# Kernel optimization log

Hardware: AMD Instinct MI355X
Metric: run time of the kernel (lower is better)

## Reference

```python
import jax, jax.numpy as jnp
import numpy as np

B, CIN, COUT, H, W = 8, 128, 128, 64, 64

# kernel-grid base offsets (dy, dx), row-major k = kh*3 + kw, matching torch base_offset-1
BASE = jnp.array([[-1, -1], [-1, 0], [-1, 1],
                  [0, -1], [0, 0], [0, 1],
                  [1, -1], [1, 0], [1, 1]], dtype=jnp.float32)  # [9,2]
CORNER = jnp.array([1, 0, 1, 0, 0, 0, 1, 0, 1], dtype=jnp.float32)  # mask1 per kernel tap
EDGE = jnp.array([0, 1, 0, 1, 0, 1, 0, 1, 0], dtype=jnp.float32)    # mask2 per kernel tap


def conv3x3(x, w, b=None):
    out = jax.lax.conv_general_dilated(
        x, w, window_strides=(1, 1), padding=((1, 1), (1, 1)),
        dimension_numbers=('NCHW', 'OIHW', 'NCHW'))
    if b is not None:
        out = out + b[None, :, None, None]
    return out


def bilinear_sample(x, py, px):
    Bv, C, Hin, Win = x.shape
    y0 = jnp.floor(py)
    x0 = jnp.floor(px)
    wy = py - y0
    wx = px - x0
    y0i = y0.astype(jnp.int32)
    x0i = x0.astype(jnp.int32)
    xf = x.reshape(Bv, C, Hin * Win)

    def corner(yi, xi):
        valid = ((yi >= 0) & (yi < Hin) & (xi >= 0) & (xi < Win)).astype(x.dtype)
        idx = jnp.clip(yi, 0, Hin - 1) * Win + jnp.clip(xi, 0, Win - 1)  # [B,K,Ho,Wo]
        g = jax.vmap(lambda xb, ib: xb[:, ib])(xf, idx)  # [B,C,K,Ho,Wo]
        return g * valid[:, None]

    v00 = corner(y0i, x0i)
    v01 = corner(y0i, x0i + 1)
    v10 = corner(y0i + 1, x0i)
    v11 = corner(y0i + 1, x0i + 1)
    wy = wy[:, None]
    wx = wx[:, None]
    return (v00 * (1 - wy) * (1 - wx) + v01 * (1 - wy) * wx
            + v10 * wy * (1 - wx) + v11 * wy * wx)


def setup_inputs() -> dict:
    key = jax.random.key(0)
    k1, k2, k3 = jax.random.split(key, 3)
    x = jax.random.normal(k1, (B, CIN, H, W), dtype=jnp.float32)
    # small offset-conv weights keep predicted offsets in a realistic sub-pixel range
    w_off = jax.random.normal(k2, (5, CIN, 3, 3), dtype=jnp.float32) * 0.02
    b_off = jnp.zeros((5,), dtype=jnp.float32)
    w = jax.random.normal(k3, (COUT, CIN, 3, 3), dtype=jnp.float32) * (1.0 / np.sqrt(CIN * 9))
    b = jnp.zeros((COUT,), dtype=jnp.float32)
    return {"x": x, "w_off": w_off, "b_off": b_off, "w": w, "b": b}


def reference(x, w_off, b_off, w, b):
    off = conv3x3(x, w_off, b_off)          # [B,5,H,W]
    scale1 = jax.nn.relu(off[:, 2:3]) + 1.0  # corner scale [B,1,H,W]
    scale2 = jax.nn.relu(off[:, 3:4]) + 1.0  # edge scale   [B,1,H,W]
    shift = off[:, :2]                       # equivariant shift vector [B,2,H,W]

    # per-tap scale; center tap gets 0 but its base offset is (0,0) anyway
    scale_k = CORNER[None, :, None, None] * scale1 + EDGE[None, :, None, None] * scale2  # [B,9,H,W]
    # deform offset = scaled_base - base + shift = base*(scale-1) + shift
    delta = BASE[None, :, :, None, None] * (scale_k - 1.0)[:, :, None] + shift[:, None]  # [B,9,2,H,W]

    hs = jnp.arange(H, dtype=x.dtype)
    ws = jnp.arange(W, dtype=x.dtype)
    # sampling positions: p0 + base_k + offset_k (stride=1, pad=1)
    py = hs[None, None, :, None] + BASE[None, :, 0, None, None] + delta[:, :, 0]  # [B,9,H,W]
    px = ws[None, None, None, :] + BASE[None, :, 1, None, None] + delta[:, :, 1]

    sampled = bilinear_sample(x, py, px)  # [B,CIN,9,H,W]
    out = jnp.einsum('bckhw,ock->bohw', sampled, w.reshape(COUT, CIN, 9))
    return out + b[None, :, None, None]
```

## Files before the change

### kernel.cpp

```cpp
#include <hip/hip_runtime.h>

#define Wd 64
#define Hd 64
#define HWp 4096
#define CIN_ 128
#define COUT_ 128

typedef _Float16 f16;
typedef _Float16 h2    __attribute__((ext_vector_type(2)));
typedef _Float16 f16x8 __attribute__((ext_vector_type(8)));
typedef float f32x4    __attribute__((ext_vector_type(4)));

__device__ inline ushort f2h(float f) {
    f16 h = (f16)f;
    return __builtin_bit_cast(ushort, h);
}
__device__ inline h2 gb(const int4& g, int d) {
    return __builtin_bit_cast(h2, (&g.x)[d]);
}
__device__ inline h2 dup(float f) {
    f16 h = (f16)f;
    h2 r; r[0] = h; r[1] = h;
    return r;
}
struct H8 { h2 r[4]; };

__global__ __launch_bounds__(256) void prep_offsets_kernel(
    const float* __restrict__ x, const float* __restrict__ w,
    const float* __restrict__ w_off, const float* __restrict__ b_off,
    ushort* __restrict__ xt, ushort* __restrict__ w_t2,
    float4* __restrict__ der)
{
    __shared__ char smem[34816];
    int blk = blockIdx.x;
    int t = threadIdx.x;

    if (blk < 256) {
        ushort* tile = (ushort*)smem;
        int b = blk >> 5, yx0 = (blk & 31) << 7;
        const float* xb = x + (size_t)b * CIN_ * HWp + yx0;
        int lanelo = t & 31, grp = t >> 5;
        #pragma unroll
        for (int i = 0; i < 4; i++) {
            int cbase = i * 32 + grp * 4;
            float4 v0 = *(const float4*)(xb + (size_t)(cbase + 0) * HWp + lanelo * 4);
            float4 v1 = *(const float4*)(xb + (size_t)(cbase + 1) * HWp + lanelo * 4);
            float4 v2 = *(const float4*)(xb + (size_t)(cbase + 2) * HWp + lanelo * 4);
            float4 v3 = *(const float4*)(xb + (size_t)(cbase + 3) * HWp + lanelo * 4);
            ushort4 u;
            u.x = f2h(v0.x); u.y = f2h(v1.x); u.z = f2h(v2.x); u.w = f2h(v3.x);
            *(ushort4*)&tile[(lanelo * 4 + 0) * 136 + cbase] = u;
            u.x = f2h(v0.y); u.y = f2h(v1.y); u.z = f2h(v2.y); u.w = f2h(v3.y);
            *(ushort4*)&tile[(lanelo * 4 + 1) * 136 + cbase] = u;
            u.x = f2h(v0.z); u.y = f2h(v1.z); u.z = f2h(v2.z); u.w = f2h(v3.z);
            *(ushort4*)&tile[(lanelo * 4 + 2) * 136 + cbase] = u;
            u.x = f2h(v0.w); u.y = f2h(v1.w); u.z = f2h(v2.w); u.w = f2h(v3.w);
            *(ushort4*)&tile[(lanelo * 4 + 3) * 136 + cbase] = u;
        }
        __syncthreads();
        ushort* dst = xt + ((size_t)b * HWp + yx0) * CIN_;
        int c8 = (t & 15) * 8, yxg = t >> 4;
        #pragma unroll
        for (int i = 0; i < 8; i++) {
            int yxl = i * 16 + yxg;
            int4 v = *(int4*)&tile[yxl * 136 + c8];
            *(int4*)(dst + (size_t)yxl * CIN_ + c8) = v;
        }
    } else if (blk < 832) {
        int i = (blk - 256) * 256 + t;
        int j    = i & 7;
        int lane = (i >> 3) & 63;
        int ii   = (i >> 9) & 3;
        int wm   = (i >> 11) & 1;
        int s    = i >> 12;
        int o = wm * 64 + ii * 16 + (lane & 15);
        int c = (s & 3) * 32 + (lane >> 4) * 8 + j;
        int k = s >> 2;
        w_t2[i] = f2h(w[o * 1152 + c * 9 + k]);
    } else {
        float* wl   = (float*)smem;
        float* part = (float*)(smem + 18432);
        int blk2 = blk - 832;
        int b = blk2 >> 6;
        int h = blk2 & 63;

        for (int i = t; i < 4608; i += 256) {
            int j = i / 1152;
            int r = i - j * 1152;
            wl[r * 4 + j] = w_off[i];
        }
        __syncthreads();

        int pi = t & 63, cc = t >> 6;
        const float* xb = x + (size_t)(b * CIN_ + cc * 32) * HWp;

        int idx9[9];
        float msk9[9];
        #pragma unroll
        for (int dy = 0; dy < 3; dy++) {
            int hy = h + dy - 1;
            int hyc = min(max(hy, 0), Hd - 1);
            bool vr = (hy >= 0) && (hy < Hd);
            #pragma unroll
            for (int dx = 0; dx < 3; dx++) {
                int wx = pi + dx - 1;
                int wxc = min(max(wx, 0), Wd - 1);
                bool v = vr && (wx >= 0) && (wx < Wd);
                idx9[dy * 3 + dx] = hyc * Wd + wxc;
                msk9[dy * 3 + dx] = v ? 1.0f : 0.0f;
            }
        }

        float o0 = 0.f, o1 = 0.f, o2 = 0.f, o3 = 0.f;
        #pragma unroll 4
        for (int c = 0; c < 32; c++) {
            const float* xp = xb + c * HWp;
            const float* wc = &wl[(cc * 32 + c) * 36];
            float xv[9];
            #pragma unroll
            for (int tp = 0; tp < 9; tp++) xv[tp] = xp[idx9[tp]] * msk9[tp];
            #pragma unroll
            for (int tp = 0; tp < 9; tp++) {
                float4 wj = *(const float4*)&wc[tp * 4];
                o0 += xv[tp] * wj.x; o1 += xv[tp] * wj.y;
                o2 += xv[tp] * wj.z; o3 += xv[tp] * wj.w;
            }
        }
        part[t * 4 + 0] = o0;
        part[t * 4 + 1] = o1;
        part[t * 4 + 2] = o2;
        part[t * 4 + 3] = o3;
        __syncthreads();

        if (t < 64) {
            float s0 = b_off[0], s1 = b_off[1], s2 = b_off[2], s3 = b_off[3];
            #pragma unroll
            for (int q = 0; q < 4; q++) {
                s0 += part[(q * 64 + t) * 4 + 0];
                s1 += part[(q * 64 + t) * 4 + 1];
                s2 += part[(q * 64 + t) * 4 + 2];
                s3 += part[(q * 64 + t) * 4 + 3];
            }
            float4 d;
            d.x = s0;
            d.y = s1;
            d.z = fmaxf(s2, 0.f) + 1.f;
            d.w = fmaxf(s3, 0.f) + 1.f;
            der[(size_t)b * HWp + h * Wd + t] = d;
        }
    }
}

__global__ __launch_bounds__(256, 3) void deform_gemm_mfma(
    const ushort* __restrict__ xt, const ushort* __restrict__ w_t2,
    const float* __restrict__ bias, const float4* __restrict__ der,
    float* __restrict__ out)
{
    __shared__ ushort A_lds[2][2][4096];
    __shared__ int4 MI[9][64];
    __shared__ int4 MW[9][64];

    int t = threadIdx.x;
    int b = blockIdx.x & 7;
    int rp = blockIdx.x >> 3;
    int p0 = rp << 6;
    const char* xtb = (const char*)(xt + (size_t)b * HWp * CIN_);

    int wv = t >> 6, lane = t & 63;
    int lm = lane & 15, lq = lane >> 4;
    int myp = wv * 16 + lm;
    int lqb = lq * 16;

    f32x4 acc[8] = {};

    {
        int p = t >> 2;
        int pg = p0 + p;
        float fh = (float)(pg >> 6), fp = (float)(pg & 63);
        float4 dv = der[(size_t)b * HWp + pg];
        for (int k = (t & 3); k < 9; k += 4) {
            int ky = (k * 11) >> 5;
            int kx = k - ky * 3;
            float by = (float)(ky - 1), bx = (float)(kx - 1);
            bool corner = (ky != 1) && (kx != 1);
            bool edge = (ky != 1) ^ (kx != 1);
            float sk = corner ? dv.z : (edge ? dv.w : 0.0f);
            float py = fh + by * sk + dv.x;
            float px = fp + bx * sk + dv.y;
            float y0f = floorf(py), x0f = floorf(px);
            float wy = py - y0f, wx = px - x0f;
            int y0 = (int)y0f, x0 = (int)x0f;
            int y1 = y0 + 1, x1 = x0 + 1;
            float vy0 = (y0 >= 0 && y0 < Hd) ? 1.f : 0.f;
            float vy1 = (y1 >= 0 && y1 < Hd) ? 1.f : 0.f;
            float vx0 = (x0 >= 0 && x0 < Wd) ? 1.f : 0.f;
            float vx1 = (x1 >= 0 && x1 < Wd) ? 1.f : 0.f;
            int cy0 = min(max(y0, 0), Hd - 1), cy1 = min(max(y1, 0), Hd - 1);
            int cx0 = min(max(x0, 0), Wd - 1), cx1 = min(max(x1, 0), Wd - 1);
            int4 ii;
            ii.x = (cy0 * Wd + cx0) << 8;
            ii.y = (cy0 * Wd + cx1) << 8;
            ii.z = (cy1 * Wd + cx0) << 8;
            ii.w = (cy1 * Wd + cx1) << 8;
            MI[k][p] = ii;
            H8 hw;
            hw.r[0] = dup((1.f - wy) * (1.f - wx) * vy0 * vx0);
            hw.r[1] = dup((1.f - wy) * wx * vy0 * vx1);
            hw.r[2] = dup(wy * (1.f - wx) * vy1 * vx0);
            hw.r[3] = dup(wy * wx * vy1 * vx1);
            MW[k][p] = __builtin_bit_cast(int4, hw);
        }
    }
    __syncthreads();

    int vo0, vo1, vo2, vo3;

    auto stageA = [&](int buf, int st) {
        const ushort* src = w_t2 + (size_t)st * 8192;
        #pragma unroll
        for (int cc = 0; cc < 2; cc++) {
            #pragma unroll
            for (int hrow = 0; hrow < 2; hrow++) {
                const ushort* g = src + cc * 4096 + (wv * 2 + hrow) * 512 + lane * 8;
                ushort* l = &A_lds[buf][cc][(wv * 2 + hrow) * 512];
                __builtin_amdgcn_global_load_lds(
                    (const __attribute__((address_space(1))) unsigned int*)g,
                    (__attribute__((address_space(3))) unsigned int*)l, 16, 0, 0);
            }
        }
    };

    auto issueG = [&](int4 (&G)[4], int qm) {
        int off = qm * 64;
        G[0] = *(const int4*)(xtb + (vo0 + off));
        G[1] = *(const int4*)(xtb + (vo1 + off));
        G[2] = *(const int4*)(xtb + (vo2 + off));
        G[3] = *(const int4*)(xtb + (vo3 + off));
    };

    auto mfmaChunk = [&](int cur, int cc, const int4 (&G)[4], const H8& cw) {
        H8 tmp;
        #pragma unroll
        for (int d = 0; d < 4; d++) {
            h2 r = gb(G[0], d) * cw.r[0];
            r = gb(G[1], d) * cw.r[1] + r;
            r = gb(G[2], d) * cw.r[2] + r;
            r = gb(G[3], d) * cw.r[3] + r;
            tmp.r[d] = r;
        }
        f16x8 bf = __builtin_bit_cast(f16x8, tmp);
        __builtin_amdgcn_s_setprio(1);
        #pragma unroll
        for (int i = 0; i < 8; i++) {
            f16x8 af = *(const f16x8*)&A_lds[cur][cc][i * 512 + lane * 8];
            acc[i] = __builtin_amdgcn_mfma_f32_16x16x32_f16(af, bf, acc[i], 0, 0, 0);
        }
        __builtin_amdgcn_s_setprio(0);
    };

    int4 GA[4], GB[4];
    H8 cwA, cwB;
    int4 idxN;

    {
        int4 mi0 = MI[0][myp];
        vo0 = mi0.x + lqb; vo1 = mi0.y + lqb; vo2 = mi0.z + lqb; vo3 = mi0.w + lqb;
        cwA = __builtin_bit_cast(H8, MW[0][myp]);
        idxN = MI[1][myp];
    }
    stageA(0, 0);
    __builtin_amdgcn_sched_barrier(0);
    issueG(GA, 0);
    asm volatile("s_waitcnt vmcnt(4)" ::: "memory");
    __builtin_amdgcn_s_barrier();
    __builtin_amdgcn_sched_barrier(0);

#define BODY(ST, CWC, CWN, DORD)                                             \
    {                                                                        \
        int cur_ = (ST) & 1, nb_ = cur_ ^ 1;                                 \
        issueG(GB, (2 * (ST) + 1) & 3);                                      \
        stageA(nb_, (ST) + 1);                                               \
        __builtin_amdgcn_sched_barrier(0);                                   \
        asm volatile("s_waitcnt vmcnt(8)" ::: "memory");                     \
        __builtin_amdgcn_sched_barrier(0);                                   \
        mfmaChunk(cur_, 0, GA, CWC);                                         \
        if (DORD) {                                                          \
            vo0 = idxN.x + lqb; vo1 = idxN.y + lqb;                          \
            vo2 = idxN.z + lqb; vo3 = idxN.w + lqb;                          \
        }                                                                    \
        issueG(GA, (2 * (ST) + 2) & 3);                                      \
        if (DORD) {                                                          \
            idxN = MI[min(((ST) >> 1) + 2, 8)][myp];                         \
            CWN  = __builtin_bit_cast(H8, MW[min(((ST) >> 1) + 1, 8)][myp]); \
        }                                                                    \
        __builtin_amdgcn_sched_barrier(0);                                   \
        asm volatile("s_waitcnt vmcnt(8)" ::: "memory");                     \
        __builtin_amdgcn_sched_barrier(0);                                   \
        mfmaChunk(cur_, 1, GB, CWC);                                         \
        asm volatile("s_waitcnt vmcnt(4)" ::: "memory");                     \
        __builtin_amdgcn_s_barrier();                                        \
        __builtin_amdgcn_sched_barrier(0);                                   \
    }

    for (int su = 0; su < 4; su++) {
        int st = su << 2;
        BODY(st,     cwA, cwB, 0);
        BODY(st + 1, cwA, cwB, 1);
        BODY(st + 2, cwB, cwA, 0);
        BODY(st + 3, cwB, cwA, 1);
    }
    BODY(16, cwA, cwB, 0);
#undef BODY

    {
        issueG(GB, 3);
        __builtin_amdgcn_sched_barrier(0);
        asm volatile("s_waitcnt vmcnt(4)" ::: "memory");
        __builtin_amdgcn_sched_barrier(0);
        mfmaChunk(1, 0, GA, cwA);
        asm volatile("s_waitcnt vmcnt(0)" ::: "memory");
        __builtin_amdgcn_sched_barrier(0);
        mfmaChunk(1, 1, GB, cwA);
    }

    int pgo = p0 + wv * 16 + lm;
    #pragma unroll
    for (int I = 0; I < 8; I++) {
        int ob = (I >> 2) * 64 + (I & 3) * 16 + lq * 4;
        #pragma unroll
        for (int r = 0; r < 4; r++) {
            int o = ob + r;
            float bv = bias[o];
            __builtin_nontemporal_store(acc[I][r] + bv,
                out + (size_t)(b * COUT_ + o) * HWp + pgo);
        }
    }
}

extern "C" void kernel_launch(void* const* d_in, const int* in_sizes, int n_in,
                              void* d_out, int out_size, void* d_ws, size_t ws_size,
                              hipStream_t stream) {
    const float* x     = (const float*)d_in[0];
    const float* w_off = (const float*)d_in[1];
    const float* b_off = (const float*)d_in[2];
    const float* w     = (const float*)d_in[3];
    const float* bias  = (const float*)d_in[4];
    float* out = (float*)d_out;

    char* ws = (char*)d_ws;
    ushort* xt   = (ushort*)ws;
    ushort* w_t2 = (ushort*)(ws + 8388608);
    float4* der  = (float4*)(ws + 8683520);

    prep_offsets_kernel<<<1344, 256, 0, stream>>>(x, w, w_off, b_off,
                                                  xt, w_t2, der);
    deform_gemm_mfma<<<512, 256, 0, stream>>>(xt, w_t2, bias, der, out);
}
```

Baseline: 131.5 us.

## Deepen gather prefetch to a full stage ahead with four register buffers

The gather loads for the bilinear corners are now issued a whole stage ahead, into four rotating register buffers, instead of one chunk ahead with two buffers. Both MFMA chunks of a stage then run back to back, with a single wait per stage. This is meant to hide more global-load latency behind the MFMA work. The extra live registers force launch bounds down from 3 to 2 blocks per CU, which lowers occupancy.

```diff
diff --git a/kernel.cpp b/kernel.cpp
--- a/kernel.cpp
+++ b/kernel.cpp
@@ -151,7 +151,7 @@
     }
 }
 
-__global__ __launch_bounds__(256, 3) void deform_gemm_mfma(
+__global__ __launch_bounds__(256, 2) void deform_gemm_mfma(
     const ushort* __restrict__ xt, const ushort* __restrict__ w_t2,
     const float* __restrict__ bias, const float4* __restrict__ der,
     float* __restrict__ out)
@@ -258,7 +258,7 @@
         __builtin_amdgcn_s_setprio(0);
     };
 
-    int4 GA[4], GB[4];
+    int4 G0[4], G1[4], G2[4], G3[4];
     H8 cwA, cwB;
     int4 idxN;
 
@@ -270,57 +270,50 @@
     }
     stageA(0, 0);
     __builtin_amdgcn_sched_barrier(0);
-    issueG(GA, 0);
-    asm volatile("s_waitcnt vmcnt(4)" ::: "memory");
+    issueG(G0, 0);
+    issueG(G1, 1);
+    __builtin_amdgcn_sched_barrier(0);
+    asm volatile("s_waitcnt vmcnt(8)" ::: "memory");
     __builtin_amdgcn_s_barrier();
     __builtin_amdgcn_sched_barrier(0);
 
-#define BODY(ST, CWC, CWN, DORD)                                             \
+#define SBODY(ST, GC0, GC1, GI0, GI1, CWC, CWN, DORD)                        \
     {                                                                        \
         int cur_ = (ST) & 1, nb_ = cur_ ^ 1;                                 \
-        issueG(GB, (2 * (ST) + 1) & 3);                                      \
         stageA(nb_, (ST) + 1);                                               \
         __builtin_amdgcn_sched_barrier(0);                                   \
-        asm volatile("s_waitcnt vmcnt(8)" ::: "memory");                     \
-        __builtin_amdgcn_sched_barrier(0);                                   \
-        mfmaChunk(cur_, 0, GA, CWC);                                         \
         if (DORD) {                                                          \
             vo0 = idxN.x + lqb; vo1 = idxN.y + lqb;                          \
             vo2 = idxN.z + lqb; vo3 = idxN.w + lqb;                          \
         }                                                                    \
-        issueG(GA, (2 * (ST) + 2) & 3);                                      \
+        issueG(GI0, (2 * (ST) + 2) & 3);                                     \
+        issueG(GI1, (2 * (ST) + 3) & 3);                                     \
         if (DORD) {                                                          \
             idxN = MI[min(((ST) >> 1) + 2, 8)][myp];                         \
             CWN  = __builtin_bit_cast(H8, MW[min(((ST) >> 1) + 1, 8)][myp]); \
         }                                                                    \
         __builtin_amdgcn_sched_barrier(0);                                   \
+        mfmaChunk(cur_, 0, GC0, CWC);                                        \
+        mfmaChunk(cur_, 1, GC1, CWC);                                        \
         asm volatile("s_waitcnt vmcnt(8)" ::: "memory");                     \
-        __builtin_amdgcn_sched_barrier(0);                                   \
-        mfmaChunk(cur_, 1, GB, CWC);                                         \
-        asm volatile("s_waitcnt vmcnt(4)" ::: "memory");                     \
         __builtin_amdgcn_s_barrier();                                        \
         __builtin_amdgcn_sched_barrier(0);                                   \
     }
 
     for (int su = 0; su < 4; su++) {
         int st = su << 2;
-        BODY(st,     cwA, cwB, 0);
-        BODY(st + 1, cwA, cwB, 1);
-        BODY(st + 2, cwB, cwA, 0);
-        BODY(st + 3, cwB, cwA, 1);
-    }
-    BODY(16, cwA, cwB, 0);
-#undef BODY
+        SBODY(st,     G0, G1, G2, G3, cwA, cwB, 0);
+        SBODY(st + 1, G2, G3, G0, G1, cwA, cwB, 1);
+        SBODY(st + 2, G0, G1, G2, G3, cwB, cwA, 0);
+        SBODY(st + 3, G2, G3, G0, G1, cwB, cwA, 1);
+    }
+    SBODY(16, G0, G1, G2, G3, cwA, cwB, 0);
+#undef SBODY
 
     {
-        issueG(GB, 3);
         __builtin_amdgcn_sched_barrier(0);
-        asm volatile("s_waitcnt vmcnt(4)" ::: "memory");
-        __builtin_amdgcn_sched_barrier(0);
-        mfmaChunk(1, 0, GA, cwA);
-        asm volatile("s_waitcnt vmcnt(0)" ::: "memory");
-        __builtin_amdgcn_sched_barrier(0);
-        mfmaChunk(1, 1, GB, cwA);
+        mfmaChunk(1, 0, G2, cwA);
+        mfmaChunk(1, 1, G3, cwA);
     }
 
     int pgo = p0 + wv * 16 + lm;
```

Measured after the change: 129.2 us. No clear change (-1.8%).
